# Kernel optimization log

Measured on AMD Instinct MI355X. Metric: run time of the kernel, lower is better.

## Reference

```python
import jax, jax.numpy as jnp
import numpy as np

ETA = 0.1      # self.eta
BETA = 0.05    # self.beta
MU = 0.05      # self.mu
MINI = 1e-6    # mini_val
SEEDS_PER_TOPIC = 10


def setup_inputs() -> dict:
    key = jax.random.key(0)
    k1, k2, k3, k4 = jax.random.split(key, 4)
    B, V, K = 64, 10000, 64
    # sparse-ish bag-of-words counts in {0,1,2}
    batch_BOW = jax.random.randint(k1, (B, V), 0, 3).astype(jnp.float32)
    # disjoint seed words: SEEDS_PER_TOPIC seed words per topic
    seeds = jnp.zeros((V, K), jnp.float32)
    rows = jnp.arange(SEEDS_PER_TOPIC * K)
    cols = jnp.repeat(jnp.arange(K), SEEDS_PER_TOPIC)
    seeds = seeds.at[rows, cols].set(1.0)
    exp_m = jax.random.uniform(k2, (B, K), jnp.float32) * 10.0     # E[m_dk] for docs in batch
    exp_s = jax.random.uniform(k3, (V, K), jnp.float32) * 5.0 * seeds  # E[s_wk], nonzero only at seed entries
    exp_n = jax.random.uniform(k4, (V, K), jnp.float32) * 5.0      # E[n_wk]
    pi = jnp.full((K,), 0.7, jnp.float32)
    return {"batch_BOW": batch_BOW, "seeds": seeds, "exp_m": exp_m,
            "exp_s": exp_s, "exp_n": exp_n, "pi": pi}


def reference(batch_BOW, seeds, exp_m, exp_s, exp_n, pi):
    # Vectorized SCVB0_guided over the whole minibatch (no per-doc Python loop).
    V, K = seeds.shape
    S = seeds.sum(0)                      # [K] number of seed words per topic
    beta_sum = BETA * V                   # self.beta_sum[guided_m]
    mu_sum = MU * S                       # [K]
    exp_s_sum = exp_s.sum(0)              # [K]
    exp_n_sum = exp_n.sum(0)              # [K]

    mask = (batch_BOW > 0).astype(batch_BOW.dtype)[:, :, None]   # [B,V,1] BOW_nonzero gather
    theta = exp_m[:, None, :] + ETA                               # [B,1,K]
    phi_s = (MU + exp_s) / (mu_sum + exp_s_sum)                   # [V,K]
    phi_n = (BETA + exp_n) / (beta_sum + exp_n_sum)               # [V,K]

    g_ss = mask * seeds[None] * theta * phi_s[None] * pi          # [B,V,K]
    g_sr = mask * seeds[None] * theta * phi_n[None] * (1.0 - pi)
    g_rr = mask * (1.0 - seeds[None]) * theta * phi_n[None]

    s_sum = g_ss.sum(-1, keepdims=True) + g_sr.sum(-1, keepdims=True)
    r_sum = g_rr.sum(-1, keepdims=True)
    g_ss = g_ss / (s_sum + MINI)
    g_sr = g_sr / (s_sum + MINI)
    g_rr = g_rr / (r_sum + MINI)

    # seed word <=> word is seed of at least one topic; else use g_rr only
    is_seed = (seeds.sum(1) > 0)[None, :, None]                   # [1,V,1]
    gamma = jnp.where(is_seed, pi * g_ss + (1.0 - pi) * (g_sr + g_rr), g_rr)

    counts = batch_BOW[:, :, None]                                # [B,V,1]
    temp_exp_m_batch = (gamma * counts).sum(1)                    # [B,K]
    temp_exp_n = ((g_sr + g_rr) * counts).sum(0)                  # [V,K] scatter-accumulate
    temp_exp_s = (g_ss * counts).sum(0)                           # [V,K]
    gamma_sr_sum = g_sr.sum((0, 1))                               # [K]
    exp_q_z = (gamma * jnp.log(gamma + MINI)).sum()               # scalar entropy term
    return temp_exp_m_batch, temp_exp_n, temp_exp_s, gamma_sr_sum, exp_q_z
```

## Files before the change

### kernel.cpp

```cpp
#include <hip/hip_runtime.h>
#include <hip/hip_bf16.h>

#define ETA_C  0.1f
#define BETA_C 0.05f
#define MU_C   0.05f
#define MINI_C 1e-6f

typedef __attribute__((ext_vector_type(8))) short short8;
typedef __attribute__((ext_vector_type(4))) float f32x4;

template<int CTRL, int ROWMASK>
__device__ __forceinline__ float dpp_add(float x) {
  int v = __builtin_amdgcn_update_dpp(0, __float_as_int(x), CTRL, ROWMASK, 0xf, true);
  return x + __int_as_float(v);
}

__device__ __forceinline__ float wave_sum(float x) {
  x = dpp_add<0xB1,  0xF>(x);
  x = dpp_add<0x4E,  0xF>(x);
  x = dpp_add<0x141, 0xF>(x);
  x = dpp_add<0x140, 0xF>(x);
  x = dpp_add<0x142, 0xA>(x);
  x = dpp_add<0x143, 0xC>(x);
  return __int_as_float(__builtin_amdgcn_readlane(__float_as_int(x), 63));
}

__device__ __forceinline__ float rl(float x, int k) {
  return __int_as_float(__builtin_amdgcn_readlane(__float_as_int(x), k));
}

__device__ __forceinline__ short bf16r(float x) {
  unsigned u = __float_as_uint(x);
  u += 0x7fffu + ((u >> 16) & 1u);
  return (short)(u >> 16);
}

__device__ __forceinline__ float bf2f(short s) {
  return __uint_as_float(((unsigned)(unsigned short)s) << 16);
}

__global__ __launch_bounds__(256) void sums_kernel(
    const float* __restrict__ seeds, const float* __restrict__ es,
    const float* __restrict__ en, float* __restrict__ part,
    float* __restrict__ out, int V, int rows_per_block, int gsr_off,
    int zeroOut) {
  __shared__ float sh[192];
  int t = threadIdx.x, bx = blockIdx.x;
  if (zeroOut) {
    if (bx < 16) out[(bx << 8) + t] = 0.f;
    else if (bx == 16 && t < 65) out[gsr_off + t] = 0.f;
  }
  if (t < 192) sh[t] = 0.f;
  __syncthreads();
  int k = t & 63, w = t >> 6;
  int v0 = bx * rows_per_block;
  int v1 = min(v0 + rows_per_block, V);
  float s0 = 0.f, s1 = 0.f, s2 = 0.f;
  for (int v = v0 + w; v < v1; v += 4) {
    int idx = (v << 6) + k;
    s0 += seeds[idx]; s1 += es[idx]; s2 += en[idx];
  }
  atomicAdd(&sh[k], s0);
  atomicAdd(&sh[64 + k], s1);
  atomicAdd(&sh[128 + k], s2);
  __syncthreads();
  if (t < 192) part[bx * 192 + t] = sh[t];
}

__global__ __launch_bounds__(1024, 4) void main_kernel(
    const float* __restrict__ bow,
    const float* __restrict__ seeds,
    const float* __restrict__ exp_m,
    const float* __restrict__ exp_s,
    const float* __restrict__ exp_n,
    const float* __restrict__ pi,
    const float* __restrict__ part,
    float* __restrict__ out,
    float* __restrict__ wsm, float* __restrict__ wsgq,
    int V, int useWs, int gsr_off, int NB) {
  __shared__ short THbf[4096];
  __shared__ short THTbf[4096];
  __shared__ short TLbf[4096];
  __shared__ short ARRT[1024];
  __shared__ short ASVT[1024];
  __shared__ short ARLT[1024];
  __shared__ short WSRT[2048];
  __shared__ short PKA[2048];
  __shared__ short CIRT[1024];
  __shared__ float RSL[64 * 17];
  __shared__ float SSL[64 * 17];
  __shared__ float L0a[64 * 17];
  __shared__ float L0b[64 * 17];
  __shared__ float sums_sh[192];
  float* NNL = RSL;
  float* red_gsr = SSL;
  float* redq = L0a;

  int t = threadIdx.x;
#pragma unroll
  for (int i = 0; i < 4; i++) {
    int idx = t + (i << 10);
    int b = idx >> 6, k = idx & 63;
    float th = exp_m[idx] + ETA_C;
    float lth = __logf(th);
    THbf[idx] = bf16r(th);
    THTbf[(k << 6) + b] = bf16r(th);
    TLbf[idx] = bf16r(th * lth);
  }
  if (t < 192) {
    float s = 0.f;
#pragma unroll 8
    for (int j = 0; j < 64; j++) s += part[j * 192 + t];
    sums_sh[t] = s;
  }
  __syncthreads();

  int lane = t & 63, w = t >> 6;
  int q = lane >> 4, c = lane & 15;
  float acc_g_tot = 0.f, acc_q_tot = 0.f;

  for (int tile = blockIdx.x; tile < NB; tile += gridDim.x) {
    int v = (tile << 4) + w;
    bool active = (v < V);

    float pik = 0.f, omp = 0.f, a_ss = 0.f, a_sr = 0.f, a_rr = 0.f;
    float bowpre = 0.f;
    bool seedRow = false;
    if (active) {
      int rbase = (v << 6) + lane;
      float seed = seeds[rbase];
      float es = exp_s[rbase];
      float en = exp_n[rbase];
      pik = pi[lane];
      float inv_ds = __builtin_amdgcn_rcpf(MU_C * sums_sh[lane] + sums_sh[64 + lane]);
      float inv_dn = __builtin_amdgcn_rcpf(BETA_C * (float)V + sums_sh[128 + lane]);
      float phi_s = (MU_C + es) * inv_ds;
      float phi_n = (BETA_C + en) * inv_dn;
      omp = 1.0f - pik;
      a_ss = seed * phi_s * pik;
      a_sr = seed * phi_n * omp;
      a_rr = (1.0f - seed) * phi_n;
      seedRow = (__ballot(seed > 0.f) != 0ull);
      float wsv = fmaf(pik, a_ss, omp * a_sr);
      float wrv = seedRow ? omp * a_rr : a_rr;
      float arrl = (a_rr > 0.f) ? a_rr * __logf(a_rr) : 0.f;
      ARRT[(w << 6) + lane] = bf16r(a_rr);
      ASVT[(w << 6) + lane] = bf16r(a_ss + a_sr);
      ARLT[(w << 6) + lane] = bf16r(arrl);
      WSRT[(lane << 5) + w] = bf16r(wsv);
      WSRT[(lane << 5) + 16 + w] = bf16r(wrv);
      bowpre = bow[lane * V + v];
    } else {
      ARRT[(w << 6) + lane] = 0;
      ASVT[(w << 6) + lane] = 0;
      ARLT[(w << 6) + lane] = 0;
      WSRT[(lane << 5) + w] = 0;
      WSRT[(lane << 5) + 16 + w] = 0;
    }
    __syncthreads();

    {
      int job = w >> 2, mt = w & 3;
      const short* Amat = (job == 3) ? TLbf : THbf;
      const short* Bmat = (job == 0) ? ARRT : (job == 1) ? ASVT
                         : (job == 2) ? ARLT : ARRT;
      float* Cd = (job == 0) ? RSL : (job == 1) ? SSL : (job == 2) ? L0a : L0b;
      f32x4 acc = {0.f, 0.f, 0.f, 0.f};
      int arow = (mt << 4) + c;
#pragma unroll
      for (int s = 0; s < 2; s++) {
        short8 af = *(const short8*)&Amat[(arow << 6) + (s << 5) + (q << 3)];
        short8 bf = *(const short8*)&Bmat[(c << 6) + (s << 5) + (q << 3)];
        acc = __builtin_amdgcn_mfma_f32_16x16x32_bf16(af, bf, acc, 0, 0, 0);
      }
#pragma unroll
      for (int r = 0; r < 4; r++)
        Cd[((mt << 4) + (q << 2) + r) * 17 + c] = acc[r];
    }
    __syncthreads();

    float acc_s = 0.f, acc_g = 0.f, acc_qk = 0.f, acc_qb = 0.f;
    if (active) {
      float rsv = RSL[lane * 17 + w];
      float ssv = SSL[lane * 17 + w];
      float ivx = __builtin_amdgcn_rcpf(ssv + MINI_C);
      float ivy = __builtin_amdgcn_rcpf(rsv + MINI_C);
      float cis = bowpre * ivx;
      float cirr = bowpre * ivy;
      PKA[(lane << 5) + w] = bf16r(cis);
      PKA[(lane << 5) + 16 + w] = bf16r(cirr);
      CIRT[(w << 6) + lane] = bf16r(cirr);
      if (!seedRow) {
        float Lb = L0a[lane * 17 + w] + L0b[lane * 17 + w];
        float q0 = (bowpre > 0.f) ? ivy : 0.f;
        float q1 = q0 * __logf(ivy);
        acc_qb = fmaf(q0, Lb, q1 * rsv);
        out[4096 + V * 64 + (v << 6) + lane] = 0.f;
      } else {
        float acc_n = 0.f;
        unsigned long long m = __ballot(bowpre > 0.f);
        while (m) {
          int b = __builtin_amdgcn_readfirstlane(__builtin_ctzll(m));
          m &= (m - 1);
          float cb = rl(bowpre, b);
          float is = rl(ivx, b), ir = rl(ivy, b);
          float th = bf2f(THbf[(b << 6) + lane]);
          float gss = th * a_ss * is;
          float gsr = th * a_sr * is;
          float grr = th * a_rr * ir;
          float gnr = gsr + grr;
          float gamma = fmaf(pik, gss, omp * gnr);
          acc_n = fmaf(gnr, cb, acc_n);
          acc_s = fmaf(gss, cb, acc_s);
          acc_g += gsr;
          acc_qk = fmaf(gamma, __logf(gamma + MINI_C), acc_qk);
        }
        out[4096 + (v << 6) + lane] = acc_n;
        out[4096 + V * 64 + (v << 6) + lane] = acc_s;
      }
    } else {
      PKA[(lane << 5) + w] = 0;
      PKA[(lane << 5) + 16 + w] = 0;
      CIRT[(w << 6) + lane] = 0;
    }
    acc_g_tot += acc_g;
    acc_q_tot += acc_qk + acc_qb;
    __syncthreads();

    {
      int tm = w >> 2, tn = w & 3;
      f32x4 acc = {0.f, 0.f, 0.f, 0.f};
      short8 af = *(const short8*)&PKA[(((tm << 4) + c) << 5) + (q << 3)];
      short8 bf = *(const short8*)&WSRT[(((tn << 4) + c) << 5) + (q << 3)];
      acc = __builtin_amdgcn_mfma_f32_16x16x32_bf16(af, bf, acc, 0, 0, 0);
#pragma unroll
      for (int r = 0; r < 4; r++) {
        int brow = (tm << 4) + (q << 2) + r;
        int kcol = (tn << 4) + c;
        float val = acc[r] * bf2f(THbf[(brow << 6) + kcol]);
        if (useWs) wsm[(size_t)tile * 4096 + (brow << 6) + kcol] = val;
        else atomicAdd(&out[(brow << 6) + kcol], val);
      }
      if (w >= 12) {
        int mt = w - 12;
        f32x4 an = {0.f, 0.f, 0.f, 0.f};
#pragma unroll
        for (int s = 0; s < 2; s++) {
          short8 a2 = *(const short8*)&THTbf[(((mt << 4) + c) << 6) + (s << 5) + (q << 3)];
          short8 b2 = *(const short8*)&CIRT[(c << 6) + (s << 5) + (q << 3)];
          an = __builtin_amdgcn_mfma_f32_16x16x32_bf16(a2, b2, an, 0, 0, 0);
        }
#pragma unroll
        for (int r = 0; r < 4; r++)
          NNL[((mt << 4) + (q << 2) + r) * 17 + c] = an[r];
      }
    }
    __syncthreads();

    if (active && !seedRow)
      out[4096 + (v << 6) + lane] = a_rr * NNL[lane * 17 + w];
  }

  __syncthreads();
  red_gsr[t] = acc_g_tot;
  float qzw = wave_sum(acc_q_tot);
  if (lane == 0) redq[w] = qzw;
  __syncthreads();

  if (w == 0) {
    float g = 0.f;
#pragma unroll
    for (int j = 0; j < 16; j++) g += red_gsr[(j << 6) + lane];
    if (useWs) wsgq[blockIdx.x * 66 + lane] = g;
    else if (g != 0.f) atomicAdd(&out[gsr_off + lane], g);
    if (t == 0) {
      float qs = 0.f;
#pragma unroll
      for (int j = 0; j < 16; j++) qs += redq[j];
      if (useWs) wsgq[blockIdx.x * 66 + 64] = qs;
      else atomicAdd(&out[gsr_off + 64], qs);
    }
  }
}

__global__ __launch_bounds__(1024) void reduce_kernel(
    const float* __restrict__ wsm, const float* __restrict__ wsgq,
    float* __restrict__ out, int NB, int NP, int gsr_off) {
  __shared__ float sh[1024];
  int t = threadIdx.x, lane = t & 63, w = t >> 6, bx = blockIdx.x;
  if (bx < 64) {
    int e = (bx << 6) + lane;
    float s0 = 0.f, s1 = 0.f, s2 = 0.f, s3 = 0.f;
    int j = w;
    for (; j + 48 < NB; j += 64) {
      s0 += wsm[(size_t)(j)      * 4096 + e];
      s1 += wsm[(size_t)(j + 16) * 4096 + e];
      s2 += wsm[(size_t)(j + 32) * 4096 + e];
      s3 += wsm[(size_t)(j + 48) * 4096 + e];
    }
    for (; j < NB; j += 16) s0 += wsm[(size_t)j * 4096 + e];
    sh[t] = (s0 + s1) + (s2 + s3);
    __syncthreads();
    if (w == 0) {
      float tot = 0.f;
#pragma unroll
      for (int i = 0; i < 16; i++) tot += sh[(i << 6) + lane];
      out[e] = tot;
    }
  } else if (bx == 64) {
    float s = 0.f;
    for (int j = w; j < NP; j += 16) s += wsgq[j * 66 + lane];
    sh[t] = s;
    __syncthreads();
    if (w == 0) {
      float tot = 0.f;
#pragma unroll
      for (int i = 0; i < 16; i++) tot += sh[(i << 6) + lane];
      out[gsr_off + lane] = tot;
    }
  } else {
    float s = 0.f;
    for (int j = t; j < NP; j += 1024) s += wsgq[j * 66 + 64];
    s = wave_sum(s);
    if (lane == 0) sh[w] = s;
    __syncthreads();
    if (t == 0) {
      float tot = 0.f;
#pragma unroll
      for (int i = 0; i < 16; i++) tot += sh[i];
      out[gsr_off + 64] = tot;
    }
  }
}

extern "C" void kernel_launch(void* const* d_in, const int* in_sizes, int n_in,
                              void* d_out, int out_size, void* d_ws,
                              size_t ws_size, hipStream_t stream) {
  (void)n_in; (void)out_size;
  const float* bow   = (const float*)d_in[0];
  const float* seeds = (const float*)d_in[1];
  const float* exp_m = (const float*)d_in[2];
  const float* exp_s = (const float*)d_in[3];
  const float* exp_n = (const float*)d_in[4];
  const float* pi    = (const float*)d_in[5];
  int K = in_sizes[5];
  int V = in_sizes[1] / K;
  float* out = (float*)d_out;
  float* ws = (float*)d_ws;

  int NB = (V + 15) / 16;
  int NP = NB < 512 ? NB : 512;
  int gsr_off = 4096 + 2 * V * 64;

  size_t needF = (size_t)NB * 4096 + (size_t)NB * 66 + 64 * 192;
  int useWs = (ws_size >= needF * 4) ? 1 : 0;

  float* wsm  = ws;
  float* wsgq = wsm + (size_t)NB * 4096;
  float* part = wsgq + (size_t)NB * 66;

  int rpb = (V + 63) / 64;
  sums_kernel<<<64, 256, 0, stream>>>(seeds, exp_s, exp_n, part, out, V, rpb,
                                      gsr_off, useWs ? 0 : 1);
  main_kernel<<<NP, 1024, 0, stream>>>(bow, seeds, exp_m, exp_s, exp_n, pi,
                                       part, out, wsm, wsgq, V, useWs, gsr_off,
                                       NB);
  if (useWs) {
    reduce_kernel<<<66, 1024, 0, stream>>>(wsm, wsgq, out, NB, NP, gsr_off);
  }
}
```

Baseline: 119.0 us.

## Accumulate MFMA partials across tiles in registers and drop the reduce kernel

The per-tile theta scaling is factored out of the tile loop, so each block keeps one MFMA accumulator across all its tiles and scales it once at the end. Results go to the output with one atomicAdd per element per block instead of per-tile workspace stores. This removes the large workspace write/read traffic and the third reduce kernel launch. The cost is heavier atomic contention on the 4096 outputs and on the gsr/entropy slots, plus nondeterministic summation order.

```diff
diff --git a/kernel.cpp b/kernel.cpp
--- a/kernel.cpp
+++ b/kernel.cpp
@@ -42,14 +42,11 @@
 __global__ __launch_bounds__(256) void sums_kernel(
     const float* __restrict__ seeds, const float* __restrict__ es,
     const float* __restrict__ en, float* __restrict__ part,
-    float* __restrict__ out, int V, int rows_per_block, int gsr_off,
-    int zeroOut) {
+    float* __restrict__ out, int V, int rows_per_block, int gsr_off) {
   __shared__ float sh[192];
   int t = threadIdx.x, bx = blockIdx.x;
-  if (zeroOut) {
-    if (bx < 16) out[(bx << 8) + t] = 0.f;
-    else if (bx == 16 && t < 65) out[gsr_off + t] = 0.f;
-  }
+  if (bx < 16) out[(bx << 8) + t] = 0.f;
+  else if (bx == 16 && t < 65) out[gsr_off + t] = 0.f;
   if (t < 192) sh[t] = 0.f;
   __syncthreads();
   int k = t & 63, w = t >> 6;
@@ -76,8 +73,7 @@
     const float* __restrict__ pi,
     const float* __restrict__ part,
     float* __restrict__ out,
-    float* __restrict__ wsm, float* __restrict__ wsgq,
-    int V, int useWs, int gsr_off, int NB) {
+    int V, int gsr_off, int NB) {
   __shared__ short THbf[4096];
   __shared__ short THTbf[4096];
   __shared__ short TLbf[4096];
@@ -118,6 +114,7 @@
   int lane = t & 63, w = t >> 6;
   int q = lane >> 4, c = lane & 15;
   float acc_g_tot = 0.f, acc_q_tot = 0.f;
+  f32x4 accP = {0.f, 0.f, 0.f, 0.f};
 
   for (int tile = blockIdx.x; tile < NB; tile += gridDim.x) {
     int v = (tile << 4) + w;
@@ -229,18 +226,9 @@
 
     {
       int tm = w >> 2, tn = w & 3;
-      f32x4 acc = {0.f, 0.f, 0.f, 0.f};
       short8 af = *(const short8*)&PKA[(((tm << 4) + c) << 5) + (q << 3)];
       short8 bf = *(const short8*)&WSRT[(((tn << 4) + c) << 5) + (q << 3)];
-      acc = __builtin_amdgcn_mfma_f32_16x16x32_bf16(af, bf, acc, 0, 0, 0);
-#pragma unroll
-      for (int r = 0; r < 4; r++) {
-        int brow = (tm << 4) + (q << 2) + r;
-        int kcol = (tn << 4) + c;
-        float val = acc[r] * bf2f(THbf[(brow << 6) + kcol]);
-        if (useWs) wsm[(size_t)tile * 4096 + (brow << 6) + kcol] = val;
-        else atomicAdd(&out[(brow << 6) + kcol], val);
-      }
+      accP = __builtin_amdgcn_mfma_f32_16x16x32_bf16(af, bf, accP, 0, 0, 0);
       if (w >= 12) {
         int mt = w - 12;
         f32x4 an = {0.f, 0.f, 0.f, 0.f};
@@ -261,6 +249,16 @@
       out[4096 + (v << 6) + lane] = a_rr * NNL[lane * 17 + w];
   }
 
+  {
+    int tm = w >> 2, tn = w & 3;
+#pragma unroll
+    for (int r = 0; r < 4; r++) {
+      int brow = (tm << 4) + (q << 2) + r;
+      int kcol = (tn << 4) + c;
+      float val = accP[r] * bf2f(THbf[(brow << 6) + kcol]);
+      atomicAdd(&out[(brow << 6) + kcol], val);
+    }
+  }
   __syncthreads();
   red_gsr[t] = acc_g_tot;
   float qzw = wave_sum(acc_q_tot);
@@ -271,64 +269,12 @@
     float g = 0.f;
 #pragma unroll
     for (int j = 0; j < 16; j++) g += red_gsr[(j << 6) + lane];
-    if (useWs) wsgq[blockIdx.x * 66 + lane] = g;
-    else if (g != 0.f) atomicAdd(&out[gsr_off + lane], g);
+    if (g != 0.f) atomicAdd(&out[gsr_off + lane], g);
     if (t == 0) {
       float qs = 0.f;
 #pragma unroll
       for (int j = 0; j < 16; j++) qs += redq[j];
-      if (useWs) wsgq[blockIdx.x * 66 + 64] = qs;
-      else atomicAdd(&out[gsr_off + 64], qs);
-    }
-  }
-}
-
-__global__ __launch_bounds__(1024) void reduce_kernel(
-    const float* __restrict__ wsm, const float* __restrict__ wsgq,
-    float* __restrict__ out, int NB, int NP, int gsr_off) {
-  __shared__ float sh[1024];
-  int t = threadIdx.x, lane = t & 63, w = t >> 6, bx = blockIdx.x;
-  if (bx < 64) {
-    int e = (bx << 6) + lane;
-    float s0 = 0.f, s1 = 0.f, s2 = 0.f, s3 = 0.f;
-    int j = w;
-    for (; j + 48 < NB; j += 64) {
-      s0 += wsm[(size_t)(j)      * 4096 + e];
-      s1 += wsm[(size_t)(j + 16) * 4096 + e];
-      s2 += wsm[(size_t)(j + 32) * 4096 + e];
-      s3 += wsm[(size_t)(j + 48) * 4096 + e];
-    }
-    for (; j < NB; j += 16) s0 += wsm[(size_t)j * 4096 + e];
-    sh[t] = (s0 + s1) + (s2 + s3);
-    __syncthreads();
-    if (w == 0) {
-      float tot = 0.f;
-#pragma unroll
-      for (int i = 0; i < 16; i++) tot += sh[(i << 6) + lane];
-      out[e] = tot;
-    }
-  } else if (bx == 64) {
-    float s = 0.f;
-    for (int j = w; j < NP; j += 16) s += wsgq[j * 66 + lane];
-    sh[t] = s;
-    __syncthreads();
-    if (w == 0) {
-      float tot = 0.f;
-#pragma unroll
-      for (int i = 0; i < 16; i++) tot += sh[(i << 6) + lane];
-      out[gsr_off + lane] = tot;
-    }
-  } else {
-    float s = 0.f;
-    for (int j = t; j < NP; j += 1024) s += wsgq[j * 66 + 64];
-    s = wave_sum(s);
-    if (lane == 0) sh[w] = s;
-    __syncthreads();
-    if (t == 0) {
-      float tot = 0.f;
-#pragma unroll
-      for (int i = 0; i < 16; i++) tot += sh[i];
-      out[gsr_off + 64] = tot;
+      atomicAdd(&out[gsr_off + 64], qs);
     }
   }
 }
@@ -336,7 +282,7 @@
 extern "C" void kernel_launch(void* const* d_in, const int* in_sizes, int n_in,
                               void* d_out, int out_size, void* d_ws,
                               size_t ws_size, hipStream_t stream) {
-  (void)n_in; (void)out_size;
+  (void)n_in; (void)out_size; (void)ws_size;
   const float* bow   = (const float*)d_in[0];
   const float* seeds = (const float*)d_in[1];
   const float* exp_m = (const float*)d_in[2];
@@ -346,26 +292,15 @@
   int K = in_sizes[5];
   int V = in_sizes[1] / K;
   float* out = (float*)d_out;
-  float* ws = (float*)d_ws;
+  float* part = (float*)d_ws;
 
   int NB = (V + 15) / 16;
   int NP = NB < 512 ? NB : 512;
   int gsr_off = 4096 + 2 * V * 64;
-
-  size_t needF = (size_t)NB * 4096 + (size_t)NB * 66 + 64 * 192;
-  int useWs = (ws_size >= needF * 4) ? 1 : 0;
-
-  float* wsm  = ws;
-  float* wsgq = wsm + (size_t)NB * 4096;
-  float* part = wsgq + (size_t)NB * 66;
-
   int rpb = (V + 63) / 64;
+
   sums_kernel<<<64, 256, 0, stream>>>(seeds, exp_s, exp_n, part, out, V, rpb,
-                                      gsr_off, useWs ? 0 : 1);
+                                      gsr_off);
   main_kernel<<<NP, 1024, 0, stream>>>(bow, seeds, exp_m, exp_s, exp_n, pi,
-                                       part, out, wsm, wsgq, V, useWs, gsr_off,
-                                       NB);
-  if (useWs) {
-    reduce_kernel<<<66, 1024, 0, stream>>>(wsm, wsgq, out, NB, NP, gsr_off);
-  }
-}
+                                       part, out, V, gsr_off, NB);
+}
```

New measurement: 111.7 us, median of 2. 1.07x faster.
